# Kernel optimization log

Hardware: AMD Instinct MI355X
Metric: run time of the kernel (lower is better)

The kernel has to match this reference:

```python
import jax, jax.numpy as jnp
import numpy as np

N_HEADS = 16
N_KV_HEADS = 4
HEAD_DIM = 128


def setup_inputs() -> dict:
    key = jax.random.key(0)
    ks = jax.random.split(key, 5)
    B, T, C = 4, 2048, 2048
    kv_dim = N_KV_HEADS * HEAD_DIM
    s = 0.02
    return {
        "x": jax.random.normal(ks[0], (B, T, C), jnp.float32),
        "Wq": jax.random.normal(ks[1], (C, C), jnp.float32) * s,
        "Wk": jax.random.normal(ks[2], (kv_dim, C), jnp.float32) * s,
        "Wv": jax.random.normal(ks[3], (kv_dim, C), jnp.float32) * s,
        "Wo": jax.random.normal(ks[4], (C, C), jnp.float32) * s,
    }


def reference(x, Wq, Wk, Wv, Wo):
    B, T, C = x.shape
    n_rep = N_HEADS // N_KV_HEADS
    # projections (nn.Linear: y = x @ W^T), reshape to (B, H, T, D)
    q = (x @ Wq.T).reshape(B, T, N_HEADS, HEAD_DIM).transpose(0, 2, 1, 3)
    k = (x @ Wk.T).reshape(B, T, N_KV_HEADS, HEAD_DIM).transpose(0, 2, 1, 3)
    v = (x @ Wv.T).reshape(B, T, N_KV_HEADS, HEAD_DIM).transpose(0, 2, 1, 3)
    # GQA: expand kv heads (repeat_interleave on head dim)
    k = jnp.repeat(k, n_rep, axis=1)
    v = jnp.repeat(v, n_rep, axis=1)
    scale = 1.0 / np.sqrt(HEAD_DIM).astype(np.float32)
    scores = jnp.einsum("bhqd,bhkd->bhqk", q, k) * scale
    causal = jnp.tril(jnp.ones((T, T), bool))
    scores = jnp.where(causal[None, None], scores, -jnp.inf)
    attn = jax.nn.softmax(scores, axis=-1)  # dropout p=0 -> identity
    out = jnp.einsum("bhqk,bhkd->bhqd", attn, v)
    out = out.transpose(0, 2, 1, 3).reshape(B, T, C)
    return out @ Wo.T
```

## Files before the change

### kernel.cpp

```cpp
#include <hip/hip_runtime.h>

#define TB 4
#define TT 2048
#define TC 2048
#define NH 16
#define NKV 4
#define HD 128
#define KVDIM (NKV*HD)
#define NQKV (TC + 2*KVDIM)
#define MTOK (TB*TT)

typedef __bf16 bf16x8 __attribute__((ext_vector_type(8)));
typedef __bf16 bf16x2 __attribute__((ext_vector_type(2)));
typedef float  f32x4  __attribute__((ext_vector_type(4)));
typedef float  f32x16 __attribute__((ext_vector_type(16)));
typedef unsigned short ushort_t;
typedef unsigned short us8 __attribute__((ext_vector_type(8)));
typedef unsigned short us4 __attribute__((ext_vector_type(4)));
typedef unsigned int u32x4 __attribute__((ext_vector_type(4)));
typedef unsigned int u32x2 __attribute__((ext_vector_type(2)));

#define QSC 0.12751743f

__device__ __forceinline__ ushort_t f2bf(float f) {
    unsigned u = __builtin_bit_cast(unsigned, f);
    u += 0x7fffu + ((u >> 16) & 1u);
    return (ushort_t)(u >> 16);
}

__device__ __forceinline__ unsigned pkbf(float lo, float hi) {
    bf16x2 v;
    v[0] = (__bf16)lo; v[1] = (__bf16)hi;
    return __builtin_bit_cast(unsigned, v);
}

__device__ __forceinline__ void gload16(const ushort_t* g, ushort_t* l) {
    __builtin_amdgcn_global_load_lds(
        (const __attribute__((address_space(1))) unsigned int*)g,
        (__attribute__((address_space(3))) unsigned int*)l, 16, 0, 0);
}

__global__ __launch_bounds__(256) void cast_all(const float* __restrict__ x,
                                                const float* __restrict__ Wq,
                                                const float* __restrict__ Wk,
                                                const float* __restrict__ Wv,
                                                const float* __restrict__ Wo,
                                                ushort_t* __restrict__ dst) {
    const long E0 = 16777216;
    const long E1 = 20971520;
    const long E2 = 22020096;
    const long E3 = 23068672;
    const long E4 = 27262976;
    long i = (long)blockIdx.x * blockDim.x + threadIdx.x;
    long stride = (long)gridDim.x * blockDim.x;
    for (long e = i * 4; e < E4; e += stride * 4) {
        const float* src; long off;
        if (e < E0)      { src = x;  off = e; }
        else if (e < E1) { src = Wq; off = e - E0; }
        else if (e < E2) { src = Wk; off = e - E1; }
        else if (e < E3) { src = Wv; off = e - E2; }
        else             { src = Wo; off = e - E3; }
        float4 v = *reinterpret_cast<const float4*>(src + off);
        us4 o;
        o[0] = f2bf(v.x); o[1] = f2bf(v.y); o[2] = f2bf(v.z); o[3] = f2bf(v.w);
        *reinterpret_cast<us4*>(dst + e) = o;
    }
}

#define LBLK 8192

template<bool OUTF32, bool QSCALE>
__global__ __launch_bounds__(512, 2) void gemm256(const ushort_t* __restrict__ A,
                                                  const ushort_t* __restrict__ Bw,
                                                  float* __restrict__ Cf,
                                                  ushort_t* __restrict__ Cb,
                                                  int M, int N, int Kd, int nbn) {
    extern __shared__ ushort_t lds[];
    const int tid = threadIdx.x;
    const int lane = tid & 63, wid = tid >> 6;
    const int wm = wid >> 2, wn = wid & 3;
    const int g = lane >> 4, l16 = lane & 15;

    const int cpx = gridDim.x >> 3;
    const int swz = (blockIdx.x & 7) * cpx + (blockIdx.x >> 3);
    const int bm = swz / nbn, bn = swz % nbn;

    const ushort_t* Ag = A  + (size_t)bm * 256 * Kd;
    const ushort_t* Bg = Bw + (size_t)bn * 256 * Kd;

    const int r0 = tid >> 3;
    const int p0 = (tid & 7) ^ (r0 & 7);
    const size_t so0 = (size_t)r0 * Kd + p0 * 8;
    const size_t so1 = so0 + (size_t)64 * Kd;
    const int ldsw0 = wid * 512;

    f32x4 acc[8][4] = {};
    bf16x8 aA[4][2], bB[2][2];

    const int NK = Kd >> 6;
    const int NI = Kd >> 7;

#define STAGE(mat, half, tile) do { if ((tile) < NK) {                                   \
    const ushort_t* sg_ = ((mat) ? Bg : Ag) + (size_t)(half) * 128 * Kd + (size_t)(tile) * 64; \
    ushort_t* lb_ = lds + (((((tile)&1)*2 + (mat))*2 + (half)) * LBLK) + ldsw0;          \
    gload16(sg_ + so0, lb_);                                                             \
    gload16(sg_ + so1, lb_ + 4096);                                                      \
} } while(0)

#define LDA(buf, qm) do {                                                                \
    const ushort_t* Ah_ = lds + (((buf)*2 + 0)*2 + wm) * LBLK;                           \
    _Pragma("unroll") for (int mi_ = 0; mi_ < 4; mi_++) {                                \
        const int r_ = (qm)*64 + mi_*16 + l16;                                           \
        _Pragma("unroll") for (int ks_ = 0; ks_ < 2; ks_++)                              \
            aA[mi_][ks_] = *reinterpret_cast<const bf16x8*>(                             \
                Ah_ + r_*64 + (((ks_*4 + g) ^ (r_ & 7)) * 8));                           \
    }                                                                                    \
} while(0)

#define LDB(buf, qn) do {                                                                \
    const ushort_t* Bh_ = lds + (((buf)*2 + 1)*2 + (wn >> 1)) * LBLK;                    \
    _Pragma("unroll") for (int nj_ = 0; nj_ < 2; nj_++) {                                \
        const int r_ = (wn & 1)*64 + (qn)*32 + nj_*16 + l16;                             \
        _Pragma("unroll") for (int ks_ = 0; ks_ < 2; ks_++)                              \
            bB[nj_][ks_] = *reinterpret_cast<const bf16x8*>(                             \
                Bh_ + r_*64 + (((ks_*4 + g) ^ (r_ & 7)) * 8));                           \
    }                                                                                    \
} while(0)

#define MM(qm, qn) do {                                                                  \
    __builtin_amdgcn_s_setprio(1);                                                       \
    _Pragma("unroll") for (int mi_ = 0; mi_ < 4; mi_++)                                  \
    _Pragma("unroll") for (int nj_ = 0; nj_ < 2; nj_++)                                  \
    _Pragma("unroll") for (int ks_ = 0; ks_ < 2; ks_++)                                  \
        acc[(qm)*4 + mi_][(qn)*2 + nj_] = __builtin_amdgcn_mfma_f32_16x16x32_bf16(       \
            aA[mi_][ks_], bB[nj_][ks_], acc[(qm)*4 + mi_][(qn)*2 + nj_], 0, 0, 0);       \
    __builtin_amdgcn_s_setprio(0);                                                       \
} while(0)

#define PH_MID() do {                                                                    \
    __builtin_amdgcn_s_barrier();                                                        \
    asm volatile("s_waitcnt lgkmcnt(0)" ::: "memory");                                   \
    __builtin_amdgcn_sched_barrier(0);                                                   \
} while(0)

#define PH_END() __builtin_amdgcn_s_barrier()
#define PH_END_VM4() do { asm volatile("s_waitcnt vmcnt(4)" ::: "memory");               \
                          __builtin_amdgcn_s_barrier(); } while(0)
#define PH_END_VM0() do { asm volatile("s_waitcnt vmcnt(0)" ::: "memory");               \
                          __builtin_amdgcn_s_barrier(); } while(0)

    STAGE(0, 0, 0); STAGE(0, 1, 0); STAGE(1, 0, 0); STAGE(1, 1, 0);
    STAGE(0, 0, 1); STAGE(0, 1, 1);
    asm volatile("s_waitcnt vmcnt(4)" ::: "memory");
    __builtin_amdgcn_s_barrier();

    for (int i = 0; i < NI; ++i) {
        const int t0 = 2 * i, t1 = 2 * i + 1;
        const bool last = (i == NI - 1);
        LDA(0, 0); LDB(0, 0);
        STAGE(1, 0, t1); STAGE(1, 1, t1);
        PH_MID(); MM(0, 0); PH_END();
        LDB(0, 1);
        PH_MID(); MM(0, 1); PH_END();
        LDA(0, 1); LDB(0, 0);
        PH_MID(); MM(1, 0); PH_END();
        LDB(0, 1);
        STAGE(0, 0, t0 + 2); STAGE(0, 1, t0 + 2);
        PH_MID(); MM(1, 1);
        if (last) PH_END_VM0(); else PH_END_VM4();
        LDA(1, 0); LDB(1, 0);
        STAGE(1, 0, t0 + 2); STAGE(1, 1, t0 + 2);
        PH_MID(); MM(0, 0); PH_END();
        LDB(1, 1);
        PH_MID(); MM(0, 1); PH_END();
        LDA(1, 1); LDB(1, 0);
        PH_MID(); MM(1, 0); PH_END();
        LDB(1, 1);
        STAGE(0, 0, t1 + 2); STAGE(0, 1, t1 + 2);
        PH_MID(); MM(1, 1);
        if (last) PH_END_VM0(); else PH_END_VM4();
    }

#pragma unroll
    for (int mi = 0; mi < 8; mi++)
#pragma unroll
        for (int nj = 0; nj < 4; nj++) {
            const int rbase = bm * 256 + wm * 128 + mi * 16 + g * 4;
            const int col   = bn * 256 + wn * 64 + nj * 16 + l16;
#pragma unroll
            for (int r = 0; r < 4; r++) {
                float v = acc[mi][nj][r];
                if (QSCALE && col < TC) v *= QSC;
                size_t off = (size_t)(rbase + r) * N + col;
                if (OUTF32) Cf[off] = v;
                else        Cb[off] = __builtin_bit_cast(ushort_t, (__bf16)v);
            }
        }
#undef STAGE
#undef LDA
#undef LDB
#undef MM
#undef PH_MID
#undef PH_END
#undef PH_END_VM4
#undef PH_END_VM0
}

__global__ __launch_bounds__(512, 2) void gemm128(const ushort_t* __restrict__ A,
                                                  const ushort_t* __restrict__ Bw,
                                                  ushort_t* __restrict__ Cb,
                                                  int N, int Kd, int nbn) {
    extern __shared__ ushort_t lds[];
    const int tid = threadIdx.x;
    const int lane = tid & 63, wid = tid >> 6;
    const int wm = wid >> 2, wn = wid & 3;
    const int g = lane >> 4, l16 = lane & 15;

    const int cpx = gridDim.x >> 3;
    const int swz = (blockIdx.x & 7) * cpx + (blockIdx.x >> 3);
    const int bm = swz / nbn, bn = swz % nbn;

    const ushort_t* Ag = A  + (size_t)bm * 128 * Kd;
    const ushort_t* Bg = Bw + (size_t)bn * 256 * Kd;

    const int r0 = tid >> 3;
    const int p0 = (tid & 7) ^ (r0 & 7);
    const size_t so0 = (size_t)r0 * Kd + p0 * 8;
    const size_t so1 = so0 + (size_t)64 * Kd;
    const int ldsw0 = wid * 512;

    f32x4 acc[4][4] = {};
    bf16x8 aA[2][2], bB[4][2];
    const int NK = Kd >> 6;

#define STG(tile, bb_) do { if ((tile) < NK) {                                           \
    const ushort_t* a_ = Ag + (size_t)(tile) * 64;                                       \
    const ushort_t* b_ = Bg + (size_t)(tile) * 64;                                       \
    gload16(a_ + so0, lds + ((bb_)*3 + 0) * 8192 + ldsw0);                               \
    gload16(a_ + so1, lds + ((bb_)*3 + 0) * 8192 + ldsw0 + 4096);                        \
    gload16(b_ + so0, lds + ((bb_)*3 + 1) * 8192 + ldsw0);                               \
    gload16(b_ + so1, lds + ((bb_)*3 + 1) * 8192 + ldsw0 + 4096);                        \
    gload16(b_ + (size_t)128 * Kd + so0, lds + ((bb_)*3 + 2) * 8192 + ldsw0);            \
    gload16(b_ + (size_t)128 * Kd + so1, lds + ((bb_)*3 + 2) * 8192 + ldsw0 + 4096);     \
} } while(0)

#define LDA1(bb, qm) do {                                                                \
    const ushort_t* Ah_ = lds + ((bb)*3 + 0) * 8192;                                     \
    _Pragma("unroll") for (int mi_ = 0; mi_ < 2; mi_++) {                                \
        const int r_ = wm*64 + (qm)*32 + mi_*16 + l16;                                   \
        _Pragma("unroll") for (int ks_ = 0; ks_ < 2; ks_++)                              \
            aA[mi_][ks_] = *reinterpret_cast<const bf16x8*>(                             \
                Ah_ + r_*64 + (((ks_*4 + g) ^ (r_ & 7)) * 8));                           \
    }                                                                                    \
} while(0)

#define LDB1(bb) do {                                                                    \
    const ushort_t* Bh_ = lds + ((bb)*3 + 1 + (wn >> 1)) * 8192;                         \
    _Pragma("unroll") for (int nj_ = 0; nj_ < 4; nj_++) {                                \
        const int r_ = (wn & 1)*64 + nj_*16 + l16;                                       \
        _Pragma("unroll") for (int ks_ = 0; ks_ < 2; ks_++)                              \
            bB[nj_][ks_] = *reinterpret_cast<const bf16x8*>(                             \
                Bh_ + r_*64 + (((ks_*4 + g) ^ (r_ & 7)) * 8));                           \
    }                                                                                    \
} while(0)

#define MM1(qm) do {                                                                     \
    __builtin_amdgcn_s_setprio(1);                                                       \
    _Pragma("unroll") for (int mi_ = 0; mi_ < 2; mi_++)                                  \
    _Pragma("unroll") for (int nj_ = 0; nj_ < 4; nj_++)                                  \
    _Pragma("unroll") for (int ks_ = 0; ks_ < 2; ks_++)                                  \
        acc[(qm)*2 + mi_][nj_] = __builtin_amdgcn_mfma_f32_16x16x32_bf16(                \
            aA[mi_][ks_], bB[nj_][ks_], acc[(qm)*2 + mi_][nj_], 0, 0, 0);                \
    __builtin_amdgcn_s_setprio(0);                                                       \
} while(0)

    STG(0, 0); STG(1, 1);
    asm volatile("s_waitcnt vmcnt(6)" ::: "memory");
    __builtin_amdgcn_s_barrier();

    int cb = 0;
    for (int t = 0; t < NK; ++t) {
        const int sb = (cb == 0) ? 2 : cb - 1;
        STG(t + 2, sb);
        LDB1(cb);
        LDA1(cb, 0);
        asm volatile("s_waitcnt lgkmcnt(0)" ::: "memory");
        __builtin_amdgcn_sched_barrier(0);
        MM1(0);
        LDA1(cb, 1);
        asm volatile("s_waitcnt lgkmcnt(0)" ::: "memory");
        __builtin_amdgcn_sched_barrier(0);
        MM1(1);
        if (t + 2 < NK) asm volatile("s_waitcnt vmcnt(6)" ::: "memory");
        else            asm volatile("s_waitcnt vmcnt(0)" ::: "memory");
        __builtin_amdgcn_s_barrier();
        cb = (cb == 2) ? 0 : cb + 1;
    }

#pragma unroll
    for (int mi = 0; mi < 4; mi++)
#pragma unroll
        for (int nj = 0; nj < 4; nj++) {
            const int rbase = bm * 128 + wm * 64 + mi * 16 + g * 4;
            const int col   = bn * 256 + wn * 64 + nj * 16 + l16;
            const float sc  = (col < TC) ? QSC : 1.f;
#pragma unroll
            for (int r = 0; r < 4; r++)
                Cb[(size_t)(rbase + r) * N + col] =
                    __builtin_bit_cast(ushort_t, (__bf16)(acc[mi][nj][r] * sc));
        }
#undef STG
#undef LDA1
#undef LDB1
#undef MM1
}

#define AQB 128
#define AKB 64
#define NTB (TT/AQB)
#define VTS 72

__global__ __launch_bounds__(256, 2) void attn_kernel(const ushort_t* __restrict__ qkv,
                                                      ushort_t* __restrict__ aout) {
    __shared__ alignas(16) ushort_t Ks[2][AKB * HD];
    __shared__ alignas(16) ushort_t Vt[2][HD * VTS];

    const int tid  = threadIdx.x;
    const int lane = tid & 63, wid = tid >> 6;
    const int hi   = lane >> 5, l31 = lane & 31;
    const int gx   = blockIdx.x;
    const int h    = blockIdx.y;
    const int b    = blockIdx.z;
    const int hk   = h >> 2;
    const size_t rowbase = (size_t)b * TT;

    const ushort_t* kg = qkv + TC + hk * HD;
    const ushort_t* vg = qkv + TC + KVDIM + hk * HD;
    const int rswz = (l31 & 7) << 3;

    us8 sk0, sk1, sk2, sk3;
    unsigned vv2[16];
    const int kr = tid >> 2, dcK = (tid & 3) * 32;
    const int vs = ((lane >> 2) & 7) << 3;

    for (int phase = 0; phase < 2; ++phase) {
        const int qb = (phase == 0 ? (NTB - 1 - gx) : gx) * AQB;
        const int q0 = qb + wid * 32;
        const int qrow = q0 + l31;

        bf16x8 qfr[8];
        {
            const ushort_t* qp = qkv + (rowbase + qrow) * NQKV + h * HD + hi * 8;
#pragma unroll
            for (int s = 0; s < 8; s++)
                qfr[s] = *reinterpret_cast<const bf16x8*>(qp + s * 16);
        }

        f32x16 oacc[4];
#pragma unroll
        for (int d = 0; d < 4; d++)
#pragma unroll
            for (int r = 0; r < 16; r++) oacc[d][r] = 0.f;
        float lsum = 0.f;

        const int ntiles = qb / AKB + 2;

        {
            const ushort_t* ksrc = kg + (rowbase + kr) * NQKV + dcK;
            sk0 = *reinterpret_cast<const us8*>(ksrc);
            sk1 = *reinterpret_cast<const us8*>(ksrc + 8);
            sk2 = *reinterpret_cast<const us8*>(ksrc + 16);
            sk3 = *reinterpret_cast<const us8*>(ksrc + 24);
            const ushort_t* vsrc = vg + (rowbase + wid * 16) * NQKV + 2 * lane;
#pragma unroll
            for (int j = 0; j < 16; j++)
                vv2[j] = *reinterpret_cast<const unsigned*>(vsrc + (size_t)j * NQKV);
        }
        if (phase) __syncthreads();

        for (int t = 0; t < ntiles; ++t) {
            const int kp0 = t * AKB;
            const int cur = t & 1;
            {
                const int kb = kr * HD + dcK, ksw = (kr & 7) << 3;
                *reinterpret_cast<us8*>(&Ks[cur][(kb     ) ^ ksw]) = sk0;
                *reinterpret_cast<us8*>(&Ks[cur][(kb +  8) ^ ksw]) = sk1;
                *reinterpret_cast<us8*>(&Ks[cur][(kb + 16) ^ ksw]) = sk2;
                *reinterpret_cast<us8*>(&Ks[cur][(kb + 24) ^ ksw]) = sk3;
                u32x4 pl0, ph0, pl1, ph1;
#pragma unroll
                for (int k = 0; k < 4; k++) {
                    pl0[k] = __builtin_amdgcn_perm(vv2[2 * k + 1], vv2[2 * k], 0x05040100u);
                    ph0[k] = __builtin_amdgcn_perm(vv2[2 * k + 1], vv2[2 * k], 0x07060302u);
                    pl1[k] = __builtin_amdgcn_perm(vv2[8 + 2 * k + 1], vv2[8 + 2 * k], 0x05040100u);
                    ph1[k] = __builtin_amdgcn_perm(vv2[8 + 2 * k + 1], vv2[8 + 2 * k], 0x07060302u);
                }
                ushort_t* r0p = &Vt[cur][(2 * lane) * VTS];
                ushort_t* r1p = &Vt[cur][(2 * lane + 1) * VTS];
                const int o0 = (wid * 16) ^ vs, o1 = (wid * 16 + 8) ^ vs;
                *reinterpret_cast<u32x4*>(r0p + o0) = pl0;
                *reinterpret_cast<u32x4*>(r0p + o1) = pl1;
                *reinterpret_cast<u32x4*>(r1p + o0) = ph0;
                *reinterpret_cast<u32x4*>(r1p + o1) = ph1;
            }
            if (t + 1 < ntiles) {
                const int kn = (t + 1) * AKB;
                const ushort_t* ksrc = kg + (rowbase + kn + kr) * NQKV + dcK;
                sk0 = *reinterpret_cast<const us8*>(ksrc);
                sk1 = *reinterpret_cast<const us8*>(ksrc + 8);
                sk2 = *reinterpret_cast<const us8*>(ksrc + 16);
                sk3 = *reinterpret_cast<const us8*>(ksrc + 24);
                const ushort_t* vsrc = vg + (rowbase + kn + wid * 16) * NQKV + 2 * lane;
#pragma unroll
                for (int j = 0; j < 16; j++)
                    vv2[j] = *reinterpret_cast<const unsigned*>(vsrc + (size_t)j * NQKV);
            }
            __syncthreads();

            if (kp0 <= q0 + 31) {
                f32x16 s0, s1;
#pragma unroll
                for (int r = 0; r < 16; r++) { s0[r] = 0.f; s1[r] = 0.f; }
                __builtin_amdgcn_s_setprio(1);
#pragma unroll
                for (int ds = 0; ds < 8; ds++) {
                    bf16x8 ka = *reinterpret_cast<const bf16x8*>(
                        &Ks[cur][(l31 * HD + ds * 16 + hi * 8) ^ rswz]);
                    s0 = __builtin_amdgcn_mfma_f32_32x32x16_bf16(ka, qfr[ds], s0, 0, 0, 0);
                }
#pragma unroll
                for (int ds = 0; ds < 8; ds++) {
                    bf16x8 ka = *reinterpret_cast<const bf16x8*>(
                        &Ks[cur][((32 + l31) * HD + ds * 16 + hi * 8) ^ rswz]);
                    s1 = __builtin_amdgcn_mfma_f32_32x32x16_bf16(ka, qfr[ds], s1, 0, 0, 0);
                }
                __builtin_amdgcn_s_setprio(0);
                if (kp0 + 63 > q0) {
#pragma unroll
                    for (int r = 0; r < 16; r++) {
                        int k0i = kp0 + (r & 3) + 8 * (r >> 2) + 4 * hi;
                        if (k0i > qrow)      s0[r] = -1e30f;
                        if (k0i + 32 > qrow) s1[r] = -1e30f;
                    }
                }
                unsigned pk0[8], pk1[8];
                float ps = 0.f;
#pragma unroll
                for (int w = 0; w < 8; w++) {
                    float a0 = exp2f(s0[2 * w]), a1 = exp2f(s0[2 * w + 1]);
                    float b0 = exp2f(s1[2 * w]), b1 = exp2f(s1[2 * w + 1]);
                    ps += (a0 + a1) + (b0 + b1);
                    pk0[w] = pkbf(a0, a1);
                    pk1[w] = pkbf(b0, b1);
                }
                ps += __shfl_xor(ps, 32);
                lsum += ps;
                __builtin_amdgcn_s_setprio(1);
#pragma unroll
                for (int ks = 0; ks < 4; ks++) {
                    const unsigned* pkt = (ks < 2) ? pk0 : pk1;
                    unsigned c00 = pkt[4 * (ks & 1) + 0];
                    unsigned c01 = pkt[4 * (ks & 1) + 1];
                    unsigned c10 = pkt[4 * (ks & 1) + 2];
                    unsigned c11 = pkt[4 * (ks & 1) + 3];
                    u32x2 rA = __builtin_amdgcn_permlane32_swap(c00, c10, false, false);
                    u32x2 rB = __builtin_amdgcn_permlane32_swap(c01, c11, false, false);
                    u32x4 faw;
                    faw[0] = rA[0];
                    faw[1] = rB[0];
                    faw[2] = rA[1];
                    faw[3] = rB[1];
                    bf16x8 pa = __builtin_bit_cast(bf16x8, faw);
#pragma unroll
                    for (int dt = 0; dt < 4; dt++) {
                        int doff = dt * 32 + l31;
                        int sr = ((doff >> 3) & 7) << 3;
                        bf16x8 vb = *reinterpret_cast<const bf16x8*>(
                            &Vt[cur][doff * VTS + ((ks * 16 + hi * 8) ^ sr)]);
                        oacc[dt] = __builtin_amdgcn_mfma_f32_32x32x16_bf16(vb, pa, oacc[dt], 0, 0, 0);
                    }
                }
                __builtin_amdgcn_s_setprio(0);
            }
        }

        const float rl = 1.f / lsum;
        ushort_t* orow = aout + (rowbase + qrow) * TC + h * HD;
#pragma unroll
        for (int dt = 0; dt < 4; dt++)
#pragma unroll
            for (int rp = 0; rp < 8; rp++) {
                int d = dt * 32 + ((2 * rp) & 3) + 8 * ((2 * rp) >> 2) + 4 * hi;
                unsigned w = pkbf(oacc[dt][2 * rp] * rl, oacc[dt][2 * rp + 1] * rl);
                *reinterpret_cast<unsigned*>(orow + d) = w;
            }
    }
}

extern "C" void kernel_launch(void* const* d_in, const int* in_sizes, int n_in,
                              void* d_out, int out_size, void* d_ws, size_t ws_size,
                              hipStream_t stream) {
    const float* x  = (const float*)d_in[0];
    const float* Wq = (const float*)d_in[1];
    const float* Wk = (const float*)d_in[2];
    const float* Wv = (const float*)d_in[3];
    const float* Wo = (const float*)d_in[4];
    float* out = (float*)d_out;

    ushort_t* x_bf  = (ushort_t*)d_ws;
    ushort_t* wqkv  = x_bf  + (size_t)MTOK * TC;
    ushort_t* wo_bf = wqkv  + (size_t)NQKV * TC;
    ushort_t* qkv   = wo_bf + (size_t)TC * TC;
    ushort_t* attn  = x_bf;

    cast_all<<<4096, 256, 0, stream>>>(x, Wq, Wk, Wv, Wo, x_bf);

    const int G128_LDS = 147456;
    const int G256_LDS = 131072;
    hipFuncSetAttribute(reinterpret_cast<const void*>(gemm128),
                        hipFuncAttributeMaxDynamicSharedMemorySize, G128_LDS);
    hipFuncSetAttribute(reinterpret_cast<const void*>(gemm256<true, false>),
                        hipFuncAttributeMaxDynamicSharedMemorySize, G256_LDS);

    gemm128<<<dim3(768), 512, G128_LDS, stream>>>(x_bf, wqkv, qkv, NQKV, TC, 12);

    attn_kernel<<<dim3(NTB / 2, NH, TB), 256, 0, stream>>>(qkv, attn);

    gemm256<true, false><<<dim3(256), 512, G256_LDS, stream>>>(
        attn, wo_bf, out, nullptr, MTOK, TC, TC, TC / 256);
}
```

Before: 323.4 us.

## Use BK=32 triple-buffered QKV GEMM and single-buffer attention LDS

The QKV projection GEMM now uses a K-tile of 32 instead of 64. That shrinks the triple-buffered LDS footprint from 144KB to 72KB and gives each iteration one fused load/MFMA phase, with more iterations and barriers overall. The kernel is templated for fp32 or bf16 output with optional Q scaling. Separately, the attention kernel drops K/V double buffering in LDS and adds a __syncthreads after each tile. This lowers its LDS use but serializes the LDS writes against the previous tile's compute.

Result: no change. 319.5 us (-1.2%).

```diff
diff --git a/kernel.cpp b/kernel.cpp
--- a/kernel.cpp
+++ b/kernel.cpp
@@ -206,10 +206,12 @@
 #undef PH_END_VM0
 }
 
-__global__ __launch_bounds__(512, 2) void gemm128(const ushort_t* __restrict__ A,
-                                                  const ushort_t* __restrict__ Bw,
-                                                  ushort_t* __restrict__ Cb,
-                                                  int N, int Kd, int nbn) {
+template<bool OUTF32, bool QSCALE>
+__global__ __launch_bounds__(512, 2) void gemm_bk32(const ushort_t* __restrict__ A,
+                                                    const ushort_t* __restrict__ Bw,
+                                                    float* __restrict__ Cf,
+                                                    ushort_t* __restrict__ Cb,
+                                                    int N, int Kd, int nbn) {
     extern __shared__ ushort_t lds[];
     const int tid = threadIdx.x;
     const int lane = tid & 63, wid = tid >> 6;
@@ -223,75 +225,59 @@
     const ushort_t* Ag = A  + (size_t)bm * 128 * Kd;
     const ushort_t* Bg = Bw + (size_t)bn * 256 * Kd;
 
-    const int r0 = tid >> 3;
-    const int p0 = (tid & 7) ^ (r0 & 7);
-    const size_t so0 = (size_t)r0 * Kd + p0 * 8;
-    const size_t so1 = so0 + (size_t)64 * Kd;
-    const int ldsw0 = wid * 512;
+    const int arow = tid >> 2;
+    const int apos = (tid & 3) ^ (arow & 3);
+    const size_t aso  = (size_t)arow * Kd + apos * 8;
+    const size_t bso0 = aso;
+    const size_t bso1 = aso + (size_t)128 * Kd;
+    const int ldsw = wid * 512;
 
     f32x4 acc[4][4] = {};
-    bf16x8 aA[2][2], bB[4][2];
-    const int NK = Kd >> 6;
-
-#define STG(tile, bb_) do { if ((tile) < NK) {                                           \
-    const ushort_t* a_ = Ag + (size_t)(tile) * 64;                                       \
-    const ushort_t* b_ = Bg + (size_t)(tile) * 64;                                       \
-    gload16(a_ + so0, lds + ((bb_)*3 + 0) * 8192 + ldsw0);                               \
-    gload16(a_ + so1, lds + ((bb_)*3 + 0) * 8192 + ldsw0 + 4096);                        \
-    gload16(b_ + so0, lds + ((bb_)*3 + 1) * 8192 + ldsw0);                               \
-    gload16(b_ + so1, lds + ((bb_)*3 + 1) * 8192 + ldsw0 + 4096);                        \
-    gload16(b_ + (size_t)128 * Kd + so0, lds + ((bb_)*3 + 2) * 8192 + ldsw0);            \
-    gload16(b_ + (size_t)128 * Kd + so1, lds + ((bb_)*3 + 2) * 8192 + ldsw0 + 4096);     \
+    bf16x8 aA[4], bB[4];
+    const int NK = Kd >> 5;
+
+#define STG(tile, bb) do { if ((tile) < NK) {                                            \
+    const ushort_t* a_ = Ag + (size_t)(tile) * 32;                                       \
+    const ushort_t* b_ = Bg + (size_t)(tile) * 32;                                       \
+    ushort_t* lb_ = lds + (bb) * 12288 + ldsw;                                           \
+    gload16(a_ + aso,  lb_);                                                             \
+    gload16(b_ + bso0, lb_ + 4096);                                                      \
+    gload16(b_ + bso1, lb_ + 8192);                                                      \
 } } while(0)
 
-#define LDA1(bb, qm) do {                                                                \
-    const ushort_t* Ah_ = lds + ((bb)*3 + 0) * 8192;                                     \
-    _Pragma("unroll") for (int mi_ = 0; mi_ < 2; mi_++) {                                \
-        const int r_ = wm*64 + (qm)*32 + mi_*16 + l16;                                   \
-        _Pragma("unroll") for (int ks_ = 0; ks_ < 2; ks_++)                              \
-            aA[mi_][ks_] = *reinterpret_cast<const bf16x8*>(                             \
-                Ah_ + r_*64 + (((ks_*4 + g) ^ (r_ & 7)) * 8));                           \
+#define LDAB(bb) do {                                                                    \
+    const ushort_t* Ah_ = lds + (bb) * 12288;                                            \
+    const ushort_t* Bh_ = Ah_ + 4096;                                                    \
+    _Pragma("unroll") for (int mi_ = 0; mi_ < 4; mi_++) {                                \
+        const int r_ = wm * 64 + mi_ * 16 + l16;                                         \
+        aA[mi_] = *reinterpret_cast<const bf16x8*>(Ah_ + r_ * 32 + ((g ^ (r_ & 3)) * 8));\
+    }                                                                                    \
+    _Pragma("unroll") for (int nj_ = 0; nj_ < 4; nj_++) {                                \
+        const int r_ = wn * 64 + nj_ * 16 + l16;                                         \
+        bB[nj_] = *reinterpret_cast<const bf16x8*>(Bh_ + r_ * 32 + ((g ^ (r_ & 3)) * 8));\
     }                                                                                    \
 } while(0)
 
-#define LDB1(bb) do {                                                                    \
-    const ushort_t* Bh_ = lds + ((bb)*3 + 1 + (wn >> 1)) * 8192;                         \
-    _Pragma("unroll") for (int nj_ = 0; nj_ < 4; nj_++) {                                \
-        const int r_ = (wn & 1)*64 + nj_*16 + l16;                                       \
-        _Pragma("unroll") for (int ks_ = 0; ks_ < 2; ks_++)                              \
-            bB[nj_][ks_] = *reinterpret_cast<const bf16x8*>(                             \
-                Bh_ + r_*64 + (((ks_*4 + g) ^ (r_ & 7)) * 8));                           \
-    }                                                                                    \
-} while(0)
-
-#define MM1(qm) do {                                                                     \
-    __builtin_amdgcn_s_setprio(1);                                                       \
-    _Pragma("unroll") for (int mi_ = 0; mi_ < 2; mi_++)                                  \
-    _Pragma("unroll") for (int nj_ = 0; nj_ < 4; nj_++)                                  \
-    _Pragma("unroll") for (int ks_ = 0; ks_ < 2; ks_++)                                  \
-        acc[(qm)*2 + mi_][nj_] = __builtin_amdgcn_mfma_f32_16x16x32_bf16(                \
-            aA[mi_][ks_], bB[nj_][ks_], acc[(qm)*2 + mi_][nj_], 0, 0, 0);                \
-    __builtin_amdgcn_s_setprio(0);                                                       \
-} while(0)
-
     STG(0, 0); STG(1, 1);
-    asm volatile("s_waitcnt vmcnt(6)" ::: "memory");
+    asm volatile("s_waitcnt vmcnt(3)" ::: "memory");
     __builtin_amdgcn_s_barrier();
 
     int cb = 0;
     for (int t = 0; t < NK; ++t) {
         const int sb = (cb == 0) ? 2 : cb - 1;
         STG(t + 2, sb);
-        LDB1(cb);
-        LDA1(cb, 0);
+        LDAB(cb);
         asm volatile("s_waitcnt lgkmcnt(0)" ::: "memory");
         __builtin_amdgcn_sched_barrier(0);
-        MM1(0);
-        LDA1(cb, 1);
-        asm volatile("s_waitcnt lgkmcnt(0)" ::: "memory");
-        __builtin_amdgcn_sched_barrier(0);
-        MM1(1);
-        if (t + 2 < NK) asm volatile("s_waitcnt vmcnt(6)" ::: "memory");
+        __builtin_amdgcn_s_setprio(1);
+#pragma unroll
+        for (int mi = 0; mi < 4; mi++)
+#pragma unroll
+            for (int nj = 0; nj < 4; nj++)
+                acc[mi][nj] = __builtin_amdgcn_mfma_f32_16x16x32_bf16(
+                    aA[mi], bB[nj], acc[mi][nj], 0, 0, 0);
+        __builtin_amdgcn_s_setprio(0);
+        if (t + 2 < NK) asm volatile("s_waitcnt vmcnt(3)" ::: "memory");
         else            asm volatile("s_waitcnt vmcnt(0)" ::: "memory");
         __builtin_amdgcn_s_barrier();
         cb = (cb == 2) ? 0 : cb + 1;
@@ -303,16 +289,17 @@
         for (int nj = 0; nj < 4; nj++) {
             const int rbase = bm * 128 + wm * 64 + mi * 16 + g * 4;
             const int col   = bn * 256 + wn * 64 + nj * 16 + l16;
-            const float sc  = (col < TC) ? QSC : 1.f;
-#pragma unroll
-            for (int r = 0; r < 4; r++)
-                Cb[(size_t)(rbase + r) * N + col] =
-                    __builtin_bit_cast(ushort_t, (__bf16)(acc[mi][nj][r] * sc));
+#pragma unroll
+            for (int r = 0; r < 4; r++) {
+                float v = acc[mi][nj][r];
+                if (QSCALE && col < TC) v *= QSC;
+                size_t off = (size_t)(rbase + r) * N + col;
+                if (OUTF32) Cf[off] = v;
+                else        Cb[off] = __builtin_bit_cast(ushort_t, (__bf16)v);
+            }
         }
 #undef STG
-#undef LDA1
-#undef LDB1
-#undef MM1
+#undef LDAB
 }
 
 #define AQB 128
@@ -322,8 +309,8 @@
 
 __global__ __launch_bounds__(256, 2) void attn_kernel(const ushort_t* __restrict__ qkv,
                                                       ushort_t* __restrict__ aout) {
-    __shared__ alignas(16) ushort_t Ks[2][AKB * HD];
-    __shared__ alignas(16) ushort_t Vt[2][HD * VTS];
+    __shared__ alignas(16) ushort_t Ks[AKB * HD];
+    __shared__ alignas(16) ushort_t Vt[HD * VTS];
 
     const int tid  = threadIdx.x;
     const int lane = tid & 63, wid = tid >> 6;
@@ -376,17 +363,15 @@
             for (int j = 0; j < 16; j++)
                 vv2[j] = *reinterpret_cast<const unsigned*>(vsrc + (size_t)j * NQKV);
         }
-        if (phase) __syncthreads();
 
         for (int t = 0; t < ntiles; ++t) {
             const int kp0 = t * AKB;
-            const int cur = t & 1;
             {
                 const int kb = kr * HD + dcK, ksw = (kr & 7) << 3;
-                *reinterpret_cast<us8*>(&Ks[cur][(kb     ) ^ ksw]) = sk0;
-                *reinterpret_cast<us8*>(&Ks[cur][(kb +  8) ^ ksw]) = sk1;
-                *reinterpret_cast<us8*>(&Ks[cur][(kb + 16) ^ ksw]) = sk2;
-                *reinterpret_cast<us8*>(&Ks[cur][(kb + 24) ^ ksw]) = sk3;
+                *reinterpret_cast<us8*>(&Ks[(kb     ) ^ ksw]) = sk0;
+                *reinterpret_cast<us8*>(&Ks[(kb +  8) ^ ksw]) = sk1;
+                *reinterpret_cast<us8*>(&Ks[(kb + 16) ^ ksw]) = sk2;
+                *reinterpret_cast<us8*>(&Ks[(kb + 24) ^ ksw]) = sk3;
                 u32x4 pl0, ph0, pl1, ph1;
 #pragma unroll
                 for (int k = 0; k < 4; k++) {
@@ -395,8 +380,8 @@
                     pl1[k] = __builtin_amdgcn_perm(vv2[8 + 2 * k + 1], vv2[8 + 2 * k], 0x05040100u);
                     ph1[k] = __builtin_amdgcn_perm(vv2[8 + 2 * k + 1], vv2[8 + 2 * k], 0x07060302u);
                 }
-                ushort_t* r0p = &Vt[cur][(2 * lane) * VTS];
-                ushort_t* r1p = &Vt[cur][(2 * lane + 1) * VTS];
+                ushort_t* r0p = &Vt[(2 * lane) * VTS];
+                ushort_t* r1p = &Vt[(2 * lane + 1) * VTS];
                 const int o0 = (wid * 16) ^ vs, o1 = (wid * 16 + 8) ^ vs;
                 *reinterpret_cast<u32x4*>(r0p + o0) = pl0;
                 *reinterpret_cast<u32x4*>(r0p + o1) = pl1;
@@ -425,13 +410,13 @@
 #pragma unroll
                 for (int ds = 0; ds < 8; ds++) {
                     bf16x8 ka = *reinterpret_cast<const bf16x8*>(
-                        &Ks[cur][(l31 * HD + ds * 16 + hi * 8) ^ rswz]);
+                        &Ks[(l31 * HD + ds * 16 + hi * 8) ^ rswz]);
                     s0 = __builtin_amdgcn_mfma_f32_32x32x16_bf16(ka, qfr[ds], s0, 0, 0, 0);
                 }
 #pragma unroll
                 for (int ds = 0; ds < 8; ds++) {
                     bf16x8 ka = *reinterpret_cast<const bf16x8*>(
-                        &Ks[cur][((32 + l31) * HD + ds * 16 + hi * 8) ^ rswz]);
+                        &Ks[((32 + l31) * HD + ds * 16 + hi * 8) ^ rswz]);
                     s1 = __builtin_amdgcn_mfma_f32_32x32x16_bf16(ka, qfr[ds], s1, 0, 0, 0);
                 }
                 __builtin_amdgcn_s_setprio(0);
@@ -476,12 +461,13 @@
                         int doff = dt * 32 + l31;
                         int sr = ((doff >> 3) & 7) << 3;
                         bf16x8 vb = *reinterpret_cast<const bf16x8*>(
-                            &Vt[cur][doff * VTS + ((ks * 16 + hi * 8) ^ sr)]);
+                            &Vt[doff * VTS + ((ks * 16 + hi * 8) ^ sr)]);
                         oacc[dt] = __builtin_amdgcn_mfma_f32_32x32x16_bf16(vb, pa, oacc[dt], 0, 0, 0);
                     }
                 }
                 __builtin_amdgcn_s_setprio(0);
             }
+            __syncthreads();
         }
 
         const float rl = 1.f / lsum;
@@ -515,14 +501,15 @@
 
     cast_all<<<4096, 256, 0, stream>>>(x, Wq, Wk, Wv, Wo, x_bf);
 
-    const int G128_LDS = 147456;
+    const int GK_LDS  = 73728;
     const int G256_LDS = 131072;
-    hipFuncSetAttribute(reinterpret_cast<const void*>(gemm128),
-                        hipFuncAttributeMaxDynamicSharedMemorySize, G128_LDS);
+    hipFuncSetAttribute(reinterpret_cast<const void*>(gemm_bk32<false, true>),
+                        hipFuncAttributeMaxDynamicSharedMemorySize, GK_LDS);
     hipFuncSetAttribute(reinterpret_cast<const void*>(gemm256<true, false>),
                         hipFuncAttributeMaxDynamicSharedMemorySize, G256_LDS);
 
-    gemm128<<<dim3(768), 512, G128_LDS, stream>>>(x_bf, wqkv, qkv, NQKV, TC, 12);
+    gemm_bk32<false, true><<<dim3(768), 512, GK_LDS, stream>>>(
+        x_bf, wqkv, nullptr, qkv, NQKV, TC, 12);
 
     attn_kernel<<<dim3(NTB / 2, NH, TB), 256, 0, stream>>>(qkv, attn);
 
```
